# Performance work log

Measured on AMD Instinct MI355X. Metric: run time of the kernel, lower is better.

Reference implementation:

```python
import jax, jax.numpy as jnp
import numpy as np
from jax import lax

T, I, H = 8192, 1024, 1024


def setup_inputs() -> dict:
    key = jax.random.key(0)
    ks = jax.random.split(key, 7)
    s = 1.0 / np.sqrt(H)
    x = jax.random.normal(ks[0], (T, I), dtype=jnp.float32)
    W_ih = jax.random.uniform(ks[1], (4 * H, I), minval=-s, maxval=s, dtype=jnp.float32)
    W_hh = jax.random.uniform(ks[2], (4 * H, H), minval=-s, maxval=s, dtype=jnp.float32)
    b_ih = jax.random.uniform(ks[3], (4 * H,), minval=-s, maxval=s, dtype=jnp.float32)
    b_hh = jax.random.uniform(ks[4], (4 * H,), minval=-s, maxval=s, dtype=jnp.float32)
    h0 = jax.random.normal(ks[5], (H,), dtype=jnp.float32)
    c0 = jax.random.uniform(ks[6], (H,), dtype=jnp.float32)
    return {"x": x, "W_ih": W_ih, "W_hh": W_hh, "b_ih": b_ih, "b_hh": b_hh, "h0": h0, "c0": c0}


def reference(x, W_ih, W_hh, b_ih, b_hh, h0, c0):
    # Precompute the input contribution to all gates in one big GEMM: [T, 4H]
    gates_x = x @ W_ih.T + (b_ih + b_hh)

    def step(carry, gx):
        h, c = carry
        g = gx + h @ W_hh.T  # [4H]
        i, f, gc, o = jnp.split(g, 4)  # PyTorch gate order: input, forget, cell, output
        i = jax.nn.sigmoid(i)
        f = jax.nn.sigmoid(f)
        gc = jnp.tanh(gc)
        o = jax.nn.sigmoid(o)
        c_new = f * c + i * gc
        h_new = o * jnp.tanh(c_new)
        return (h_new, c_new), h_new

    (_, _), hs = lax.scan(step, (h0, c0), gates_x)
    return hs  # [T, H] — the per-timestep outputs collected in fullDataOutput
```

## Files before the change

kernel.cpp:

```cpp
#include <hip/hip_runtime.h>
#include <cstdint>

#define T_STEPS 8192
#define HDIM    1024
#define NBLK    256
#define NTHR    256

typedef float        f32x4 __attribute__((ext_vector_type(4)));
typedef unsigned int u32x4 __attribute__((ext_vector_type(4)));

__device__ __forceinline__ float dot4(f32x4 a, f32x4 b) {
    return a[0] * b[0] + a[1] * b[1] + a[2] * b[2] + a[3] * b[3];
}
__device__ __forceinline__ float sigmoidf_(float v) { return 1.0f / (1.0f + __expf(-v)); }
__device__ __forceinline__ float tanhf_(float v)    { return 1.0f - 2.0f / (__expf(2.0f * v) + 1.0f); }

__global__ __launch_bounds__(NTHR, 1)
void lstm_persistent(const float* __restrict__ x,
                     const float* __restrict__ W_ih,
                     const float* __restrict__ W_hh,
                     const float* __restrict__ b_ih,
                     const float* __restrict__ b_hh,
                     const float* __restrict__ h0,
                     const float* __restrict__ c0,
                     float* __restrict__ out,
                     unsigned long long* __restrict__ ring)
{
    __shared__ float h_lds[2][HDIM];

    const int tid = threadIdx.x;
    const int w   = tid >> 6;
    const int l   = tid & 63;
    const int u   = (blockIdx.x << 2) + w;

    f32x4 whh[16], wih[16];
#pragma unroll
    for (int q = 0; q < 4; ++q) {
        const float* rh = W_hh + (size_t)(q * HDIM + u) * HDIM + 4 * l;
        const float* ri = W_ih + (size_t)(q * HDIM + u) * HDIM + 4 * l;
#pragma unroll
        for (int i = 0; i < 4; ++i) {
            whh[q * 4 + i] = *(const f32x4*)(rh + 256 * i);
            wih[q * 4 + i] = *(const f32x4*)(ri + 256 * i);
        }
    }
#pragma unroll
    for (int k = 0; k < 16; ++k) {
        asm volatile("" : "+v"(whh[k]));
        asm volatile("" : "+v"(wih[k]));
    }

    float bias[4];
#pragma unroll
    for (int q = 0; q < 4; ++q) bias[q] = b_ih[q * HDIM + u] + b_hh[q * HDIM + u];
    float c = c0[u];

    f32x4 hr[4];
#pragma unroll
    for (int i = 0; i < 4; ++i) hr[i] = *(const f32x4*)(h0 + 4 * l + 256 * i);

    float gxp[4];
    {
        f32x4 x0[4];
#pragma unroll
        for (int i = 0; i < 4; ++i) x0[i] = *(const f32x4*)(x + 4 * l + 256 * i);
#pragma unroll
        for (int q = 0; q < 4; ++q) {
            float a = 0.f;
#pragma unroll
            for (int i = 0; i < 4; ++i) a += dot4(wih[q * 4 + i], x0[i]);
            gxp[q] = a;
        }
    }
    f32x4 xr[4], xn[4];
#pragma unroll
    for (int i = 0; i < 4; ++i) xr[i] = *(const f32x4*)(x + HDIM + 4 * l + 256 * i);

    for (int t = 0; t < T_STEPS; ++t) {
        float acc[4];
#pragma unroll
        for (int q = 0; q < 4; ++q) {
            float a = gxp[q];
#pragma unroll
            for (int i = 0; i < 4; ++i) a += dot4(whh[q * 4 + i], hr[i]);
            acc[q] = a;
        }
#pragma unroll
        for (int m = 1; m < 64; m <<= 1) {
#pragma unroll
            for (int q = 0; q < 4; ++q) acc[q] += __shfl_xor(acc[q], m, 64);
        }
        const float gi = sigmoidf_(acc[0] + bias[0]);
        const float gf = sigmoidf_(acc[1] + bias[1]);
        const float gg = tanhf_   (acc[2] + bias[2]);
        const float go = sigmoidf_(acc[3] + bias[3]);
        c = gf * c + gi * gg;
        const float hval = go * tanhf_(c);

        if (l == 0) {
            const unsigned long long pk =
                ((unsigned long long)(unsigned)(t + 1) << 32) |
                (unsigned long long)__float_as_uint(hval);
            __hip_atomic_store(&ring[(t & 1) * HDIM + u], pk,
                               __ATOMIC_RELAXED, __HIP_MEMORY_SCOPE_AGENT);
            out[(size_t)t * HDIM + u] = hval;
        }
        if (t == T_STEPS - 1) break;

        {
            const int tn = (t + 2 < T_STEPS) ? (t + 2) : (T_STEPS - 1);
            const float* xp = x + (size_t)tn * HDIM;
#pragma unroll
            for (int i = 0; i < 4; ++i) xn[i] = *(const f32x4*)(xp + 4 * l + 256 * i);
        }
#pragma unroll
        for (int q = 0; q < 4; ++q) {
            float a = 0.f;
#pragma unroll
            for (int i = 0; i < 4; ++i) a += dot4(wih[q * 4 + i], xr[i]);
            gxp[q] = a;
        }

        {
            const unsigned e = (unsigned)(t + 1);
            const unsigned long long base =
                (unsigned long long)(ring + (t & 1) * HDIM + 4 * tid);
            u32x4 p0, p1;
            for (;;) {
                asm volatile(
                    "global_load_dwordx4 %0, %2, off sc0 sc1\n\t"
                    "global_load_dwordx4 %1, %2, off offset:16 sc0 sc1\n\t"
                    "s_waitcnt vmcnt(0)"
                    : "=&v"(p0), "=&v"(p1)
                    : "v"(base)
                    : "memory");
                if (p0[1] == e && p0[3] == e && p1[1] == e && p1[3] == e) break;
            }
            const int ns = (t + 1) & 1;
            f32x4 hv;
            hv[0] = __uint_as_float(p0[0]);
            hv[1] = __uint_as_float(p0[2]);
            hv[2] = __uint_as_float(p1[0]);
            hv[3] = __uint_as_float(p1[2]);
            *(f32x4*)&h_lds[ns][4 * tid] = hv;
        }
        __syncthreads();
        {
            const int ns = (t + 1) & 1;
#pragma unroll
            for (int i = 0; i < 4; ++i)
                hr[i] = *(const f32x4*)&h_lds[ns][4 * l + 256 * i];
        }
#pragma unroll
        for (int i = 0; i < 4; ++i) xr[i] = xn[i];
    }
}

extern "C" void kernel_launch(void* const* d_in, const int* in_sizes, int n_in,
                              void* d_out, int out_size, void* d_ws, size_t ws_size,
                              hipStream_t stream)
{
    const float* x    = (const float*)d_in[0];
    const float* W_ih = (const float*)d_in[1];
    const float* W_hh = (const float*)d_in[2];
    const float* b_ih = (const float*)d_in[3];
    const float* b_hh = (const float*)d_in[4];
    const float* h0   = (const float*)d_in[5];
    const float* c0   = (const float*)d_in[6];

    unsigned long long* ring = (unsigned long long*)d_ws;
    hipMemsetAsync(d_ws, 0, 2 * HDIM * sizeof(unsigned long long), stream);
    lstm_persistent<<<NBLK, NTHR, 0, stream>>>(x, W_ih, W_hh, b_ih, b_hh, h0, c0,
                                               (float*)d_out, ring);
}
```

Before: 23.40 ms.

## Precompute input gate projections with a separate GEMM before the recurrent loop

```diff
diff --git a/kernel.cpp b/kernel.cpp
--- a/kernel.cpp
+++ b/kernel.cpp
@@ -3,8 +3,6 @@
 
 #define T_STEPS 8192
 #define HDIM    1024
-#define NBLK    256
-#define NTHR    256
 
 typedef float        f32x4 __attribute__((ext_vector_type(4)));
 typedef unsigned int u32x4 __attribute__((ext_vector_type(4)));
@@ -15,16 +13,62 @@
 __device__ __forceinline__ float sigmoidf_(float v) { return 1.0f / (1.0f + __expf(-v)); }
 __device__ __forceinline__ float tanhf_(float v)    { return 1.0f - 2.0f / (__expf(2.0f * v) + 1.0f); }
 
-__global__ __launch_bounds__(NTHR, 1)
-void lstm_persistent(const float* __restrict__ x,
-                     const float* __restrict__ W_ih,
-                     const float* __restrict__ W_hh,
-                     const float* __restrict__ b_ih,
-                     const float* __restrict__ b_hh,
-                     const float* __restrict__ h0,
-                     const float* __restrict__ c0,
-                     float* __restrict__ out,
-                     unsigned long long* __restrict__ ring)
+__global__ __launch_bounds__(256)
+void gemm_gx(const float* __restrict__ x, const float* __restrict__ W_ih,
+             const float* __restrict__ b_ih, const float* __restrict__ b_hh,
+             float* __restrict__ gxT)
+{
+    __shared__ float a_s[16][68];
+    __shared__ float b_s[16][68];
+    const int t  = threadIdx.x;
+    const int bm = blockIdx.x >> 6;
+    const int bn = blockIdx.x & 63;
+    const int m0 = bm << 6, n0 = bn << 6;
+    const int tx = t & 15, ty = t >> 4;
+    const int lm = t >> 2;
+    const int lk = (t & 3) << 2;
+
+    float acc[4][4] = {};
+    for (int k0 = 0; k0 < 1024; k0 += 16) {
+        f32x4 av = *(const f32x4*)(x    + (size_t)(m0 + lm) * 1024 + k0 + lk);
+        f32x4 bv = *(const f32x4*)(W_ih + (size_t)(n0 + lm) * 1024 + k0 + lk);
+        __syncthreads();
+#pragma unroll
+        for (int j = 0; j < 4; ++j) { a_s[lk + j][lm] = av[j]; b_s[lk + j][lm] = bv[j]; }
+        __syncthreads();
+#pragma unroll
+        for (int k = 0; k < 16; ++k) {
+            f32x4 af = *(const f32x4*)&a_s[k][4 * ty];
+            f32x4 bf = *(const f32x4*)&b_s[k][4 * tx];
+#pragma unroll
+            for (int i = 0; i < 4; ++i)
+#pragma unroll
+                for (int j = 0; j < 4; ++j) acc[i][j] += af[i] * bf[j];
+        }
+    }
+    f32x4 bi = *(const f32x4*)&b_ih[n0 + 4 * tx];
+    f32x4 bh = *(const f32x4*)&b_hh[n0 + 4 * tx];
+#pragma unroll
+    for (int j = 0; j < 4; ++j) {
+        const int n = n0 + 4 * tx + j;
+        const float bias = bi[j] + bh[j];
+        const int q = n >> 10, cidx = n & 1023;
+        const int bg = cidx >> 2, r = cidx & 3;
+#pragma unroll
+        for (int i = 0; i < 4; ++i) {
+            const int m = m0 + 4 * ty + i;
+            gxT[((size_t)bg * T_STEPS + m) * 16 + q * 4 + r] = acc[i][j] + bias;
+        }
+    }
+}
+
+__global__ __launch_bounds__(256, 1)
+void lstm_loop(const float* __restrict__ W_hh,
+               const float* __restrict__ h0,
+               const float* __restrict__ c0,
+               const float* __restrict__ gxT,
+               float* __restrict__ out,
+               unsigned long long* __restrict__ ring)
 {
     __shared__ float h_lds[2][HDIM];
 
@@ -33,55 +77,35 @@
     const int l   = tid & 63;
     const int u   = (blockIdx.x << 2) + w;
 
-    f32x4 whh[16], wih[16];
+    f32x4 whh[16];
 #pragma unroll
     for (int q = 0; q < 4; ++q) {
         const float* rh = W_hh + (size_t)(q * HDIM + u) * HDIM + 4 * l;
-        const float* ri = W_ih + (size_t)(q * HDIM + u) * HDIM + 4 * l;
-#pragma unroll
-        for (int i = 0; i < 4; ++i) {
-            whh[q * 4 + i] = *(const f32x4*)(rh + 256 * i);
-            wih[q * 4 + i] = *(const f32x4*)(ri + 256 * i);
-        }
-    }
-#pragma unroll
-    for (int k = 0; k < 16; ++k) {
-        asm volatile("" : "+v"(whh[k]));
-        asm volatile("" : "+v"(wih[k]));
-    }
-
-    float bias[4];
-#pragma unroll
-    for (int q = 0; q < 4; ++q) bias[q] = b_ih[q * HDIM + u] + b_hh[q * HDIM + u];
+#pragma unroll
+        for (int i = 0; i < 4; ++i) whh[q * 4 + i] = *(const f32x4*)(rh + 256 * i);
+    }
+    asm volatile("" : "+v"(whh[0]), "+v"(whh[1]), "+v"(whh[2]), "+v"(whh[3]),
+                      "+v"(whh[4]), "+v"(whh[5]), "+v"(whh[6]), "+v"(whh[7]),
+                      "+v"(whh[8]), "+v"(whh[9]), "+v"(whh[10]), "+v"(whh[11]),
+                      "+v"(whh[12]), "+v"(whh[13]), "+v"(whh[14]), "+v"(whh[15]));
+
     float c = c0[u];
-
     f32x4 hr[4];
 #pragma unroll
     for (int i = 0; i < 4; ++i) hr[i] = *(const f32x4*)(h0 + 4 * l + 256 * i);
 
-    float gxp[4];
-    {
-        f32x4 x0[4];
-#pragma unroll
-        for (int i = 0; i < 4; ++i) x0[i] = *(const f32x4*)(x + 4 * l + 256 * i);
+    const float* gxb = gxT + (size_t)blockIdx.x * T_STEPS * 16;
+    const int le = l & 15;
+    float gxA = gxb[le];
+    float gxB = gxb[16 + le];
+    float gxC = 0.f;
+
+    for (int t = 0; t < T_STEPS; ++t) {
+        float acc[4];
 #pragma unroll
         for (int q = 0; q < 4; ++q) {
             float a = 0.f;
 #pragma unroll
-            for (int i = 0; i < 4; ++i) a += dot4(wih[q * 4 + i], x0[i]);
-            gxp[q] = a;
-        }
-    }
-    f32x4 xr[4], xn[4];
-#pragma unroll
-    for (int i = 0; i < 4; ++i) xr[i] = *(const f32x4*)(x + HDIM + 4 * l + 256 * i);
-
-    for (int t = 0; t < T_STEPS; ++t) {
-        float acc[4];
-#pragma unroll
-        for (int q = 0; q < 4; ++q) {
-            float a = gxp[q];
-#pragma unroll
             for (int i = 0; i < 4; ++i) a += dot4(whh[q * 4 + i], hr[i]);
             acc[q] = a;
         }
@@ -90,10 +114,10 @@
 #pragma unroll
             for (int q = 0; q < 4; ++q) acc[q] += __shfl_xor(acc[q], m, 64);
         }
-        const float gi = sigmoidf_(acc[0] + bias[0]);
-        const float gf = sigmoidf_(acc[1] + bias[1]);
-        const float gg = tanhf_   (acc[2] + bias[2]);
-        const float go = sigmoidf_(acc[3] + bias[3]);
+        const float gi = sigmoidf_(acc[0] + __shfl(gxA, 0 + w, 64));
+        const float gf = sigmoidf_(acc[1] + __shfl(gxA, 4 + w, 64));
+        const float gg = tanhf_   (acc[2] + __shfl(gxA, 8 + w, 64));
+        const float go = sigmoidf_(acc[3] + __shfl(gxA, 12 + w, 64));
         c = gf * c + gi * gg;
         const float hval = go * tanhf_(c);
 
@@ -109,16 +133,7 @@
 
         {
             const int tn = (t + 2 < T_STEPS) ? (t + 2) : (T_STEPS - 1);
-            const float* xp = x + (size_t)tn * HDIM;
-#pragma unroll
-            for (int i = 0; i < 4; ++i) xn[i] = *(const f32x4*)(xp + 4 * l + 256 * i);
-        }
-#pragma unroll
-        for (int q = 0; q < 4; ++q) {
-            float a = 0.f;
-#pragma unroll
-            for (int i = 0; i < 4; ++i) a += dot4(wih[q * 4 + i], xr[i]);
-            gxp[q] = a;
+            gxC = gxb[(size_t)tn * 16 + le];
         }
 
         {
@@ -135,6 +150,128 @@
                     : "v"(base)
                     : "memory");
                 if (p0[1] == e && p0[3] == e && p1[1] == e && p1[3] == e) break;
+                __builtin_amdgcn_s_sleep(1);
+            }
+            const int ns = (t + 1) & 1;
+            f32x4 hv;
+            hv[0] = __uint_as_float(p0[0]);
+            hv[1] = __uint_as_float(p0[2]);
+            hv[2] = __uint_as_float(p1[0]);
+            hv[3] = __uint_as_float(p1[2]);
+            *(f32x4*)&h_lds[ns][4 * tid] = hv;
+        }
+        __syncthreads();
+        {
+            const int ns = (t + 1) & 1;
+#pragma unroll
+            for (int i = 0; i < 4; ++i)
+                hr[i] = *(const f32x4*)&h_lds[ns][4 * l + 256 * i];
+        }
+        gxA = gxB; gxB = gxC;
+    }
+}
+
+__global__ __launch_bounds__(256, 1)
+void lstm_fb(const float* __restrict__ x, const float* __restrict__ W_ih,
+             const float* __restrict__ W_hh, const float* __restrict__ b_ih,
+             const float* __restrict__ b_hh, const float* __restrict__ h0,
+             const float* __restrict__ c0, float* __restrict__ out,
+             unsigned long long* __restrict__ ring)
+{
+    __shared__ float h_lds[2][HDIM];
+    const int tid = threadIdx.x, w = tid >> 6, l = tid & 63;
+    const int u = (blockIdx.x << 2) + w;
+
+    f32x4 whh[16], wih[16];
+#pragma unroll
+    for (int q = 0; q < 4; ++q) {
+        const float* rh = W_hh + (size_t)(q * HDIM + u) * HDIM + 4 * l;
+        const float* ri = W_ih + (size_t)(q * HDIM + u) * HDIM + 4 * l;
+#pragma unroll
+        for (int i = 0; i < 4; ++i) {
+            whh[q * 4 + i] = *(const f32x4*)(rh + 256 * i);
+            wih[q * 4 + i] = *(const f32x4*)(ri + 256 * i);
+        }
+    }
+    float bias[4];
+#pragma unroll
+    for (int q = 0; q < 4; ++q) bias[q] = b_ih[q * HDIM + u] + b_hh[q * HDIM + u];
+    float c = c0[u];
+    f32x4 hr[4];
+#pragma unroll
+    for (int i = 0; i < 4; ++i) hr[i] = *(const f32x4*)(h0 + 4 * l + 256 * i);
+
+    float gxp[4];
+    {
+        f32x4 x0[4];
+#pragma unroll
+        for (int i = 0; i < 4; ++i) x0[i] = *(const f32x4*)(x + 4 * l + 256 * i);
+#pragma unroll
+        for (int q = 0; q < 4; ++q) {
+            float a = 0.f;
+#pragma unroll
+            for (int i = 0; i < 4; ++i) a += dot4(wih[q * 4 + i], x0[i]);
+            gxp[q] = a;
+        }
+    }
+    f32x4 xr[4], xn[4];
+#pragma unroll
+    for (int i = 0; i < 4; ++i) xr[i] = *(const f32x4*)(x + HDIM + 4 * l + 256 * i);
+
+    for (int t = 0; t < T_STEPS; ++t) {
+        float acc[4];
+#pragma unroll
+        for (int q = 0; q < 4; ++q) {
+            float a = gxp[q];
+#pragma unroll
+            for (int i = 0; i < 4; ++i) a += dot4(whh[q * 4 + i], hr[i]);
+            acc[q] = a;
+        }
+#pragma unroll
+        for (int m = 1; m < 64; m <<= 1) {
+#pragma unroll
+            for (int q = 0; q < 4; ++q) acc[q] += __shfl_xor(acc[q], m, 64);
+        }
+        const float gi = sigmoidf_(acc[0] + bias[0]);
+        const float gf = sigmoidf_(acc[1] + bias[1]);
+        const float gg = tanhf_   (acc[2] + bias[2]);
+        const float go = sigmoidf_(acc[3] + bias[3]);
+        c = gf * c + gi * gg;
+        const float hval = go * tanhf_(c);
+        if (l == 0) {
+            const unsigned long long pk =
+                ((unsigned long long)(unsigned)(t + 1) << 32) |
+                (unsigned long long)__float_as_uint(hval);
+            __hip_atomic_store(&ring[(t & 1) * HDIM + u], pk,
+                               __ATOMIC_RELAXED, __HIP_MEMORY_SCOPE_AGENT);
+            out[(size_t)t * HDIM + u] = hval;
+        }
+        if (t == T_STEPS - 1) break;
+        {
+            const int tn = (t + 2 < T_STEPS) ? (t + 2) : (T_STEPS - 1);
+            const float* xp = x + (size_t)tn * HDIM;
+#pragma unroll
+            for (int i = 0; i < 4; ++i) xn[i] = *(const f32x4*)(xp + 4 * l + 256 * i);
+        }
+#pragma unroll
+        for (int q = 0; q < 4; ++q) {
+            float a = 0.f;
+#pragma unroll
+            for (int i = 0; i < 4; ++i) a += dot4(wih[q * 4 + i], xr[i]);
+            gxp[q] = a;
+        }
+        {
+            const unsigned e = (unsigned)(t + 1);
+            const unsigned long long base =
+                (unsigned long long)(ring + (t & 1) * HDIM + 4 * tid);
+            u32x4 p0, p1;
+            for (;;) {
+                asm volatile(
+                    "global_load_dwordx4 %0, %2, off sc0 sc1\n\t"
+                    "global_load_dwordx4 %1, %2, off offset:16 sc0 sc1\n\t"
+                    "s_waitcnt vmcnt(0)"
+                    : "=&v"(p0), "=&v"(p1) : "v"(base) : "memory");
+                if (p0[1] == e && p0[3] == e && p1[1] == e && p1[3] == e) break;
             }
             const int ns = (t + 1) & 1;
             f32x4 hv;
@@ -170,6 +307,14 @@
 
     unsigned long long* ring = (unsigned long long*)d_ws;
     hipMemsetAsync(d_ws, 0, 2 * HDIM * sizeof(unsigned long long), stream);
-    lstm_persistent<<<NBLK, NTHR, 0, stream>>>(x, W_ih, W_hh, b_ih, b_hh, h0, c0,
-                                               (float*)d_out, ring);
-}
+
+    const size_t need = (size_t)(1u << 20) + (size_t)256 * T_STEPS * 16 * sizeof(float);
+    if (ws_size >= need) {
+        float* gxT = (float*)((char*)d_ws + (1u << 20));
+        gemm_gx<<<8192, 256, 0, stream>>>(x, W_ih, b_ih, b_hh, gxT);
+        lstm_loop<<<256, 256, 0, stream>>>(W_hh, h0, c0, gxT, (float*)d_out, ring);
+    } else {
+        lstm_fb<<<256, 256, 0, stream>>>(x, W_ih, W_hh, b_ih, b_hh, h0, c0,
+                                         (float*)d_out, ring);
+    }
+}
```

New measurement: 29.43 ms. 25.8% more time.

## Hoist input projection into a separate GEMM and stage W_hh in LDS

Applied to the files above, without the earlier changes.

```diff
diff --git a/kernel.cpp b/kernel.cpp
--- a/kernel.cpp
+++ b/kernel.cpp
@@ -3,8 +3,6 @@
 
 #define T_STEPS 8192
 #define HDIM    1024
-#define NBLK    256
-#define NTHR    256
 
 typedef float        f32x4 __attribute__((ext_vector_type(4)));
 typedef unsigned int u32x4 __attribute__((ext_vector_type(4)));
@@ -15,17 +13,64 @@
 __device__ __forceinline__ float sigmoidf_(float v) { return 1.0f / (1.0f + __expf(-v)); }
 __device__ __forceinline__ float tanhf_(float v)    { return 1.0f - 2.0f / (__expf(2.0f * v) + 1.0f); }
 
-__global__ __launch_bounds__(NTHR, 1)
-void lstm_persistent(const float* __restrict__ x,
-                     const float* __restrict__ W_ih,
-                     const float* __restrict__ W_hh,
-                     const float* __restrict__ b_ih,
-                     const float* __restrict__ b_hh,
-                     const float* __restrict__ h0,
-                     const float* __restrict__ c0,
-                     float* __restrict__ out,
-                     unsigned long long* __restrict__ ring)
+__global__ __launch_bounds__(256)
+void gemm_gx(const float* __restrict__ x, const float* __restrict__ W_ih,
+             const float* __restrict__ b_ih, const float* __restrict__ b_hh,
+             float* __restrict__ gxT)
 {
+    __shared__ float a_s[16][68];
+    __shared__ float b_s[16][68];
+    const int t  = threadIdx.x;
+    const int bm = blockIdx.x >> 6;
+    const int bn = blockIdx.x & 63;
+    const int m0 = bm << 6, n0 = bn << 6;
+    const int tx = t & 15, ty = t >> 4;
+    const int lm = t >> 2;
+    const int lk = (t & 3) << 2;
+
+    float acc[4][4] = {};
+    for (int k0 = 0; k0 < 1024; k0 += 16) {
+        f32x4 av = *(const f32x4*)(x    + (size_t)(m0 + lm) * 1024 + k0 + lk);
+        f32x4 bv = *(const f32x4*)(W_ih + (size_t)(n0 + lm) * 1024 + k0 + lk);
+        __syncthreads();
+#pragma unroll
+        for (int j = 0; j < 4; ++j) { a_s[lk + j][lm] = av[j]; b_s[lk + j][lm] = bv[j]; }
+        __syncthreads();
+#pragma unroll
+        for (int k = 0; k < 16; ++k) {
+            f32x4 af = *(const f32x4*)&a_s[k][4 * ty];
+            f32x4 bf = *(const f32x4*)&b_s[k][4 * tx];
+#pragma unroll
+            for (int i = 0; i < 4; ++i)
+#pragma unroll
+                for (int j = 0; j < 4; ++j) acc[i][j] += af[i] * bf[j];
+        }
+    }
+    f32x4 bi = *(const f32x4*)&b_ih[n0 + 4 * tx];
+    f32x4 bh = *(const f32x4*)&b_hh[n0 + 4 * tx];
+#pragma unroll
+    for (int j = 0; j < 4; ++j) {
+        const int n = n0 + 4 * tx + j;
+        const float bias = bi[j] + bh[j];
+        const int q = n >> 10, cidx = n & 1023;
+        const int bg = cidx >> 2, r = cidx & 3;
+#pragma unroll
+        for (int i = 0; i < 4; ++i) {
+            const int m = m0 + 4 * ty + i;
+            gxT[((size_t)bg * T_STEPS + m) * 16 + q * 4 + r] = acc[i][j] + bias;
+        }
+    }
+}
+
+__global__ __launch_bounds__(256)
+void lstm_loop(const float* __restrict__ W_hh,
+               const float* __restrict__ h0,
+               const float* __restrict__ c0,
+               const float* __restrict__ gxT,
+               float* __restrict__ out,
+               unsigned long long* __restrict__ ring)
+{
+    __shared__ float whh_lds[16 * HDIM];
     __shared__ float h_lds[2][HDIM];
 
     const int tid = threadIdx.x;
@@ -33,56 +78,40 @@
     const int l   = tid & 63;
     const int u   = (blockIdx.x << 2) + w;
 
-    f32x4 whh[16], wih[16];
-#pragma unroll
-    for (int q = 0; q < 4; ++q) {
-        const float* rh = W_hh + (size_t)(q * HDIM + u) * HDIM + 4 * l;
-        const float* ri = W_ih + (size_t)(q * HDIM + u) * HDIM + 4 * l;
-#pragma unroll
-        for (int i = 0; i < 4; ++i) {
-            whh[q * 4 + i] = *(const f32x4*)(rh + 256 * i);
-            wih[q * 4 + i] = *(const f32x4*)(ri + 256 * i);
-        }
-    }
 #pragma unroll
     for (int k = 0; k < 16; ++k) {
-        asm volatile("" : "+v"(whh[k]));
-        asm volatile("" : "+v"(wih[k]));
+        const int c   = tid + (k << 8);
+        const int row = c >> 8;
+        const int e4  = c & 255;
+        const int ww  = row >> 2, q = row & 3;
+        const int uu  = (blockIdx.x << 2) + ww;
+        f32x4 v = *(const f32x4*)(W_hh + (size_t)(q * HDIM + uu) * HDIM + 4 * e4);
+        *(f32x4*)&whh_lds[(ww * 4 + q) * HDIM + 4 * e4] = v;
     }
 
-    float bias[4];
-#pragma unroll
-    for (int q = 0; q < 4; ++q) bias[q] = b_ih[q * HDIM + u] + b_hh[q * HDIM + u];
     float c = c0[u];
-
     f32x4 hr[4];
 #pragma unroll
     for (int i = 0; i < 4; ++i) hr[i] = *(const f32x4*)(h0 + 4 * l + 256 * i);
 
-    float gxp[4];
-    {
-        f32x4 x0[4];
-#pragma unroll
-        for (int i = 0; i < 4; ++i) x0[i] = *(const f32x4*)(x + 4 * l + 256 * i);
-#pragma unroll
-        for (int q = 0; q < 4; ++q) {
-            float a = 0.f;
-#pragma unroll
-            for (int i = 0; i < 4; ++i) a += dot4(wih[q * 4 + i], x0[i]);
-            gxp[q] = a;
-        }
-    }
-    f32x4 xr[4], xn[4];
-#pragma unroll
-    for (int i = 0; i < 4; ++i) xr[i] = *(const f32x4*)(x + HDIM + 4 * l + 256 * i);
+    const float* gxb = gxT + (size_t)blockIdx.x * T_STEPS * 16;
+    const int le = l & 15;
+    float gxA = gxb[le];
+    float gxB = gxb[16 + le];
+    float gxC = 0.f;
+
+    __syncthreads();
+
+    const float* wl = &whh_lds[(w * 4) * HDIM + 4 * l];
 
     for (int t = 0; t < T_STEPS; ++t) {
         float acc[4];
 #pragma unroll
         for (int q = 0; q < 4; ++q) {
-            float a = gxp[q];
+            float a = 0.f;
 #pragma unroll
-            for (int i = 0; i < 4; ++i) a += dot4(whh[q * 4 + i], hr[i]);
+            for (int i = 0; i < 4; ++i)
+                a += dot4(*(const f32x4*)&wl[q * HDIM + 256 * i], hr[i]);
             acc[q] = a;
         }
 #pragma unroll
@@ -90,10 +119,10 @@
 #pragma unroll
             for (int q = 0; q < 4; ++q) acc[q] += __shfl_xor(acc[q], m, 64);
         }
-        const float gi = sigmoidf_(acc[0] + bias[0]);
-        const float gf = sigmoidf_(acc[1] + bias[1]);
-        const float gg = tanhf_   (acc[2] + bias[2]);
-        const float go = sigmoidf_(acc[3] + bias[3]);
+        const float gi = sigmoidf_(acc[0] + __shfl(gxA, 0 + w, 64));
+        const float gf = sigmoidf_(acc[1] + __shfl(gxA, 4 + w, 64));
+        const float gg = tanhf_   (acc[2] + __shfl(gxA, 8 + w, 64));
+        const float go = sigmoidf_(acc[3] + __shfl(gxA, 12 + w, 64));
         c = gf * c + gi * gg;
         const float hval = go * tanhf_(c);
 
@@ -101,24 +130,16 @@
             const unsigned long long pk =
                 ((unsigned long long)(unsigned)(t + 1) << 32) |
                 (unsigned long long)__float_as_uint(hval);
-            __hip_atomic_store(&ring[(t & 1) * HDIM + u], pk,
-                               __ATOMIC_RELAXED, __HIP_MEMORY_SCOPE_AGENT);
+            asm volatile("global_store_dwordx2 %0, %1, off sc0 sc1"
+                         :: "v"((unsigned long long)&ring[(t & 1) * HDIM + u]),
+                            "v"(pk) : "memory");
             out[(size_t)t * HDIM + u] = hval;
         }
         if (t == T_STEPS - 1) break;
 
         {
             const int tn = (t + 2 < T_STEPS) ? (t + 2) : (T_STEPS - 1);
-            const float* xp = x + (size_t)tn * HDIM;
-#pragma unroll
-            for (int i = 0; i < 4; ++i) xn[i] = *(const f32x4*)(xp + 4 * l + 256 * i);
-        }
-#pragma unroll
-        for (int q = 0; q < 4; ++q) {
-            float a = 0.f;
-#pragma unroll
-            for (int i = 0; i < 4; ++i) a += dot4(wih[q * 4 + i], xr[i]);
-            gxp[q] = a;
+            gxC = gxb[(size_t)tn * 16 + le];
         }
 
         {
@@ -132,8 +153,7 @@
                     "global_load_dwordx4 %1, %2, off offset:16 sc0 sc1\n\t"
                     "s_waitcnt vmcnt(0)"
                     : "=&v"(p0), "=&v"(p1)
-                    : "v"(base)
-                    : "memory");
+                    : "v"(base));
                 if (p0[1] == e && p0[3] == e && p1[1] == e && p1[3] == e) break;
             }
             const int ns = (t + 1) & 1;
@@ -151,8 +171,7 @@
             for (int i = 0; i < 4; ++i)
                 hr[i] = *(const f32x4*)&h_lds[ns][4 * l + 256 * i];
         }
-#pragma unroll
-        for (int i = 0; i < 4; ++i) xr[i] = xn[i];
+        gxA = gxB; gxB = gxC;
     }
 }
 
@@ -169,7 +188,9 @@
     const float* c0   = (const float*)d_in[6];
 
     unsigned long long* ring = (unsigned long long*)d_ws;
+    float* gxT = (float*)((char*)d_ws + (1u << 20));
+
     hipMemsetAsync(d_ws, 0, 2 * HDIM * sizeof(unsigned long long), stream);
-    lstm_persistent<<<NBLK, NTHR, 0, stream>>>(x, W_ih, W_hh, b_ih, b_hh, h0, c0,
-                                               (float*)d_out, ring);
+    gemm_gx<<<8192, 256, 0, stream>>>(x, W_ih, b_ih, b_hh, gxT);
+    lstm_loop<<<256, 256, 0, stream>>>(W_hh, h0, c0, gxT, (float*)d_out, ring);
 }
```

After: 31.46 ms. 34.5% more time.
